# Kernel tuning notes

Hardware: AMD Instinct MI355X
Metric: run time of the kernel (lower is better)

Reference implementation:

```python
import jax, jax.numpy as jnp
import numpy as np

B, S, D, H, E = 2, 2048, 1024, 2048, 8
TOP_K = 2
AUX_COEF = 0.01


def setup_inputs() -> dict:
    key = jax.random.key(0)
    ks = jax.random.split(key, 5)
    x = jax.random.normal(ks[0], (B, S, D), jnp.float32)
    Wr = jax.random.normal(ks[1], (E, D), jnp.float32) * 0.02   # router: Linear(D, E) weight [E, D]
    W1 = jax.random.normal(ks[2], (E, H, D), jnp.float32) * 0.02  # per-expert Linear(D, H)
    W2 = jax.random.normal(ks[3], (E, D, H), jnp.float32) * 0.02  # per-expert Linear(H, D)
    W3 = jax.random.normal(ks[4], (E, H, D), jnp.float32) * 0.02  # per-expert Linear(D, H)
    return {"x": x, "Wr": Wr, "W1": W1, "W2": W2, "W3": W3}


def reference(x, Wr, W1, W2, W3):
    b, s, d = x.shape
    e = Wr.shape[0]
    xf = x.reshape(-1, d)                               # [N, D]
    logits = xf @ Wr.T                                  # [N, E]
    probs = jax.nn.softmax(logits, axis=-1)
    _, topk_idx = jax.lax.top_k(logits, TOP_K)          # indices from logits (as in torch code)
    topk_probs, _ = jax.lax.top_k(probs, TOP_K)         # values from probs (same order; softmax monotone)
    # aux loss: density of top-1 expert * mean router prob
    density = jnp.mean(jax.nn.one_hot(topk_idx[:, 0], e, dtype=xf.dtype), axis=0)
    aux_loss = AUX_COEF * jnp.sum(density * probs.mean(axis=0)) * e
    # combine gates: gate[n, j] = sum_i topk_probs[n,i] * 1[topk_idx[n,i]==j]
    gates = jnp.sum(jax.nn.one_hot(topk_idx, e, dtype=xf.dtype) * topk_probs[..., None], axis=1)  # [N, E]
    # dense per-expert SwiGLU; masked combine gives identical math to gather/scatter loop
    h = jax.nn.silu(jnp.einsum('nd,ehd->enh', xf, W1)) * jnp.einsum('nd,ehd->enh', xf, W3)  # [E, N, H]
    y = jnp.einsum('enh,edh->end', h, W2)               # [E, N, D]
    out = jnp.einsum('ne,end->nd', gates, y)            # [N, D]
    return out.reshape(b, s, d), aux_loss
```

## Files before the change

### kernel.cpp

```cpp
#include <hip/hip_runtime.h>
#include <stdint.h>

#define NTOK 4096
#define DD 1024
#define HH 2048
#define NE 8
#define CAP 4096

typedef short bf16x8 __attribute__((ext_vector_type(8)));
typedef float f32x4 __attribute__((ext_vector_type(4)));
typedef unsigned short u16;
typedef unsigned int u32;

__device__ __forceinline__ u16 f2b(float f){
    union { float f; u32 u; } v; v.f = f;
    return (u16)((v.u + 0x7fffu + ((v.u >> 16) & 1u)) >> 16);
}
__device__ __forceinline__ float b2f(u16 h){
    union { u32 u; float f; } v; v.u = ((u32)h) << 16;
    return v.f;
}
__device__ __forceinline__ u32 pk2(float a, float b){
    return (u32)f2b(a) | ((u32)f2b(b) << 16);
}
__device__ __forceinline__ void gload16(const u16* g, u16* l){
    __builtin_amdgcn_global_load_lds((const __attribute__((address_space(1))) u32*)g,
                                     (__attribute__((address_space(3))) u32*)l, 16, 0, 0);
}

__global__ __launch_bounds__(256) void prep_kernel(const float* __restrict__ x,
        const float* __restrict__ Wr,
        const float* __restrict__ W1, const float* __restrict__ W2, const float* __restrict__ W3,
        u16* __restrict__ xb, u16* __restrict__ w1b, u16* __restrict__ w2b, u16* __restrict__ w3b,
        int* __restrict__ cnt, int* __restrict__ list,
        float* __restrict__ glist, float* __restrict__ psum,
        int* __restrict__ cnt1, int* __restrict__ islot){
    __shared__ float wS[NE * DD];
    __shared__ float psumS[NE];
    __shared__ int cnt1S[NE], cntS[NE], baseS[NE];
    __shared__ int tE[32], tL[32];
    __shared__ float tP[32];
    int tid = threadIdx.x;
    int bid = blockIdx.x;

    if (bid >= 256){
        int cb = bid - 256;
        int m = cb >> 10, blk = cb & 1023;
        const float* s = (m == 0) ? W1 : (m == 1) ? W2 : W3;
        u16* d = (m == 0) ? w1b : (m == 1) ? w2b : w3b;
        int base = blk * 4096 + tid;
        #pragma unroll 4
        for (int j = 0; j < 16; ++j){
            int i = base + j * 256;
            float4 v = reinterpret_cast<const float4*>(s)[i];
            ushort4 o; o.x = f2b(v.x); o.y = f2b(v.y); o.z = f2b(v.z); o.w = f2b(v.w);
            reinterpret_cast<ushort4*>(d)[i] = o;
        }
        return;
    }

    for (int i = tid; i < NE * DD / 4; i += 256)
        reinterpret_cast<float4*>(wS)[i] = reinterpret_cast<const float4*>(Wr)[i];
    if (tid < NE){ psumS[tid] = 0.f; cnt1S[tid] = 0; cntS[tid] = 0; }
    __syncthreads();
    int lane = tid & 63, w = tid >> 6;
    for (int t = 0; t < 4; ++t){
        int li = w * 4 + t;
        int n = bid * 16 + li;
        const float4* xr = reinterpret_cast<const float4*>(x + (size_t)n * DD);
        ushort4* xbr = reinterpret_cast<ushort4*>(xb + (size_t)n * DD);
        float acc[NE];
        #pragma unroll
        for (int e = 0; e < NE; ++e) acc[e] = 0.f;
        #pragma unroll
        for (int j = 0; j < 4; ++j){
            float4 xv = xr[lane + 64 * j];
            ushort4 xo; xo.x = f2b(xv.x); xo.y = f2b(xv.y); xo.z = f2b(xv.z); xo.w = f2b(xv.w);
            xbr[lane + 64 * j] = xo;
            #pragma unroll
            for (int e = 0; e < NE; ++e){
                float4 wv = reinterpret_cast<const float4*>(wS + e * DD)[lane + 64 * j];
                acc[e] += xv.x * wv.x + xv.y * wv.y + xv.z * wv.z + xv.w * wv.w;
            }
        }
        #pragma unroll
        for (int e = 0; e < NE; ++e){
            float v = acc[e];
            #pragma unroll
            for (int s = 32; s > 0; s >>= 1) v += __shfl_xor(v, s);
            acc[e] = v;
        }
        if (lane == 0){
            float mx = acc[0];
            #pragma unroll
            for (int e = 1; e < NE; ++e) mx = fmaxf(mx, acc[e]);
            float p[NE], sm = 0.f;
            #pragma unroll
            for (int e = 0; e < NE; ++e){ p[e] = expf(acc[e] - mx); sm += p[e]; }
            float inv = 1.f / sm;
            #pragma unroll
            for (int e = 0; e < NE; ++e){ p[e] *= inv; atomicAdd(&psumS[e], p[e]); }
            int i0 = 0;
            #pragma unroll
            for (int e = 1; e < NE; ++e) if (acc[e] > acc[i0]) i0 = e;
            int i1 = -1;
            #pragma unroll
            for (int e = 0; e < NE; ++e) if (e != i0 && (i1 < 0 || acc[e] > acc[i1])) i1 = e;
            atomicAdd(&cnt1S[i0], 1);
            int l0 = atomicAdd(&cntS[i0], 1);
            int l1 = atomicAdd(&cntS[i1], 1);
            tE[li * 2] = i0; tE[li * 2 + 1] = i1;
            tP[li * 2] = p[i0]; tP[li * 2 + 1] = p[i1];
            tL[li * 2] = l0; tL[li * 2 + 1] = l1;
        }
    }
    __syncthreads();
    if (tid < NE){
        baseS[tid] = atomicAdd(&cnt[tid], cntS[tid]);
        atomicAdd(&psum[tid], psumS[tid]);
        atomicAdd(&cnt1[tid], cnt1S[tid]);
    }
    __syncthreads();
    if (tid < 32){
        int e = tE[tid], pos = baseS[e] + tL[tid];
        int n = bid * 16 + (tid >> 1);
        list[e * CAP + pos]  = n;
        glist[e * CAP + pos] = tP[tid];
        islot[n * 2 + (tid & 1)] = e * CAP + pos;
    }
}

__global__ void finalize_kernel(const int* __restrict__ cnt, int* __restrict__ offs,
                                const float* __restrict__ psum, const int* __restrict__ cnt1,
                                float* __restrict__ aux_out){
    if (threadIdx.x == 0 && blockIdx.x == 0){
        int o = 0; float aux = 0.f;
        for (int e = 0; e < NE; ++e){
            offs[e] = o; o += cnt[e];
            aux += ((float)cnt1[e] * (1.f / NTOK)) * (psum[e] * (1.f / NTOK));
        }
        aux_out[0] = 0.01f * aux * (float)NE;
    }
}

__global__ __launch_bounds__(256, 3) void ffn1_kernel(const u16* __restrict__ xb,
        const u16* __restrict__ w1b, const u16* __restrict__ w3b,
        const int* __restrict__ cnt, const int* __restrict__ offs,
        const int* __restrict__ list, u16* __restrict__ hbuf){
    int bid = blockIdx.x;
    int widx = (bid & 7) * 1024 + (bid >> 3);
    int e = widx >> 10, n0t = (widx >> 5) & 31, mt = widx & 31;
    int rows = cnt[e];
    int m0 = mt * 128;
    if (m0 >= rows) return;
    int n0 = n0t * 64;

    __shared__ u16 aS[128 * 64];
    __shared__ u16 bS[128 * 64];

    int tid = threadIdx.x, lane = tid & 63, w = tid >> 6;
    int wm = (w & 1) * 64, wn = (w >> 1) * 32;
    int fr = lane & 15, fg = lane >> 4, fr7 = fr & 7;
    int rc = lane >> 3, ce = ((lane & 7) ^ rc) * 8;

    const u16* aptr[4];
    const u16* bptr[4];
    #pragma unroll
    for (int q = 0; q < 4; ++q){
        int r = m0 + (w * 4 + q) * 8 + rc;
        int tok = list[e * CAP + (r < rows ? r : rows - 1)];
        aptr[q] = xb + (size_t)tok * DD + ce;
        int br = (w * 4 + q) * 8 + rc;
        const u16* wb = (br < 64) ? w1b : w3b;
        bptr[q] = wb + ((size_t)e * HH + n0 + (br & 63)) * DD + ce;
    }
    u16* aL = aS + w * 4 * 512;
    u16* bL = bS + w * 4 * 512;

    f32x4 acc1[4][2], acc3[4][2];
    #pragma unroll
    for (int mi = 0; mi < 4; ++mi)
        #pragma unroll
        for (int ni = 0; ni < 2; ++ni)
            #pragma unroll
            for (int j = 0; j < 4; ++j){ acc1[mi][ni][j] = 0.f; acc3[mi][ni][j] = 0.f; }

    for (int k0 = 0; k0 < DD; k0 += 64){
        #pragma unroll
        for (int q = 0; q < 4; ++q){
            gload16(aptr[q] + k0, aL + q * 512);
            gload16(bptr[q] + k0, bL + q * 512);
        }
        __syncthreads();
        #pragma unroll
        for (int ks = 0; ks < 2; ++ks){
            int sl = ((ks * 4 + fg) ^ fr7) * 8;
            bf16x8 a[4], b1[2], b3[2];
            #pragma unroll
            for (int mi = 0; mi < 4; ++mi)
                a[mi] = *reinterpret_cast<const bf16x8*>(&aS[(wm + mi * 16 + fr) * 64 + sl]);
            #pragma unroll
            for (int ni = 0; ni < 2; ++ni){
                b1[ni] = *reinterpret_cast<const bf16x8*>(&bS[(wn + ni * 16 + fr) * 64 + sl]);
                b3[ni] = *reinterpret_cast<const bf16x8*>(&bS[(64 + wn + ni * 16 + fr) * 64 + sl]);
            }
            #pragma unroll
            for (int mi = 0; mi < 4; ++mi)
                #pragma unroll
                for (int ni = 0; ni < 2; ++ni){
                    acc1[mi][ni] = __builtin_amdgcn_mfma_f32_16x16x32_bf16(a[mi], b1[ni], acc1[mi][ni], 0, 0, 0);
                    acc3[mi][ni] = __builtin_amdgcn_mfma_f32_16x16x32_bf16(a[mi], b3[ni], acc3[mi][ni], 0, 0, 0);
                }
        }
        __syncthreads();
    }

    int hoff = offs[e];
    #pragma unroll
    for (int mi = 0; mi < 4; ++mi)
        #pragma unroll
        for (int ni = 0; ni < 2; ++ni)
            #pragma unroll
            for (int j = 0; j < 4; ++j){
                int r = wm + mi * 16 + fg * 4 + j;
                int tr = m0 + r;
                if (tr < rows){
                    int c = n0 + wn + ni * 16 + fr;
                    float v1 = acc1[mi][ni][j], v3 = acc3[mi][ni][j];
                    float hv = (v1 / (1.f + expf(-v1))) * v3;
                    hbuf[(size_t)(hoff + tr) * HH + c] = f2b(hv);
                }
            }
}

__global__ __launch_bounds__(256, 3) void ffn2_kernel(const u16* __restrict__ hbuf,
        const u16* __restrict__ w2b, const int* __restrict__ cnt,
        const int* __restrict__ offs, u16* __restrict__ ybuf){
    int bid = blockIdx.x;
    int widx = (bid & 7) * 256 + (bid >> 3);
    int e = widx >> 8, n0t = (widx >> 5) & 7, mt = widx & 31;
    int rows = cnt[e];
    int m0 = mt * 128;
    if (m0 >= rows) return;
    int n0 = n0t * 128;

    __shared__ u16 aS[128 * 64];
    __shared__ u16 bS[128 * 64];

    int tid = threadIdx.x, lane = tid & 63, w = tid >> 6;
    int wm = (w & 1) * 64, wn = (w >> 1) * 64;
    int fr = lane & 15, fg = lane >> 4, fr7 = fr & 7;
    int rc = lane >> 3, ce = ((lane & 7) ^ rc) * 8;

    int hoff = offs[e];
    const u16* aptr[4];
    #pragma unroll
    for (int q = 0; q < 4; ++q){
        int r = m0 + (w * 4 + q) * 8 + rc;
        if (r >= rows) r = rows - 1;
        aptr[q] = hbuf + (size_t)(hoff + r) * HH + ce;
    }
    const u16* bp = w2b + ((size_t)e * DD + n0 + w * 32 + rc) * HH + ce;
    u16* aL = aS + w * 4 * 512;
    u16* bL = bS + w * 4 * 512;

    f32x4 acc[4][4];
    #pragma unroll
    for (int mi = 0; mi < 4; ++mi)
        #pragma unroll
        for (int ni = 0; ni < 4; ++ni)
            #pragma unroll
            for (int j = 0; j < 4; ++j) acc[mi][ni][j] = 0.f;

    for (int k0 = 0; k0 < HH; k0 += 64){
        #pragma unroll
        for (int q = 0; q < 4; ++q){
            gload16(aptr[q] + k0, aL + q * 512);
            gload16(bp + q * 8 * HH + k0, bL + q * 512);
        }
        __syncthreads();
        #pragma unroll
        for (int ks = 0; ks < 2; ++ks){
            int sl = ((ks * 4 + fg) ^ fr7) * 8;
            bf16x8 a[4], b[4];
            #pragma unroll
            for (int mi = 0; mi < 4; ++mi)
                a[mi] = *reinterpret_cast<const bf16x8*>(&aS[(wm + mi * 16 + fr) * 64 + sl]);
            #pragma unroll
            for (int ni = 0; ni < 4; ++ni)
                b[ni] = *reinterpret_cast<const bf16x8*>(&bS[(wn + ni * 16 + fr) * 64 + sl]);
            #pragma unroll
            for (int mi = 0; mi < 4; ++mi)
                #pragma unroll
                for (int ni = 0; ni < 4; ++ni)
                    acc[mi][ni] = __builtin_amdgcn_mfma_f32_16x16x32_bf16(a[mi], b[ni], acc[mi][ni], 0, 0, 0);
        }
        __syncthreads();
    }

    #pragma unroll
    for (int mi = 0; mi < 4; ++mi)
        #pragma unroll
        for (int ni = 0; ni < 4; ++ni)
            #pragma unroll
            for (int j = 0; j < 4; ++j){
                int r = wm + mi * 16 + fg * 4 + j;
                int tr = m0 + r;
                if (tr < rows){
                    int c = wn + ni * 16 + fr;
                    ybuf[(size_t)(hoff + tr) * DD + n0 + c] = f2b(acc[mi][ni][j]);
                }
            }
}

__global__ __launch_bounds__(256, 2) void ffn1_small(const u16* __restrict__ xb,
        const float* __restrict__ W1f, const float* __restrict__ W3f,
        const int* __restrict__ cnt, const int* __restrict__ offs,
        const int* __restrict__ list, u16* __restrict__ hbuf){
    int bid = blockIdx.x;
    int widx = (bid & 7) * 512 + (bid >> 3);
    int e = widx >> 9, n0t = (widx >> 5) & 15, mt = widx & 31;
    int rows = cnt[e];
    int m0 = mt * 128;
    if (m0 >= rows) return;
    int n0 = n0t * 128;
    __shared__ u16 aS[128 * 64];
    __shared__ u16 b1S[128 * 64];
    __shared__ u16 b3S[128 * 64];
    int tid = threadIdx.x, lane = tid & 63, w = tid >> 6;
    int wm = (w & 1) * 64, wn = (w >> 1) * 64;
    int fr = lane & 15, fg = lane >> 4, fr7 = fr & 7;
    int rc = lane >> 3, ce = ((lane & 7) ^ rc) * 8;
    const u16* aptr[4];
    #pragma unroll
    for (int q = 0; q < 4; ++q){
        int r = m0 + (w * 4 + q) * 8 + rc;
        int tok = list[e * CAP + (r < rows ? r : rows - 1)];
        aptr[q] = xb + (size_t)tok * DD + ce;
    }
    size_t brw = (size_t)(e * HH + n0 + w * 32 + rc) * DD + ce;
    const float* b1pf = W1f + brw;
    const float* b3pf = W3f + brw;
    u16* aL  = aS  + w * 4 * 512;
    u16* b1L = b1S + w * 4 * 512;
    u16* b3L = b3S + w * 4 * 512;
    f32x4 acc1[4][4], acc3[4][4];
    #pragma unroll
    for (int mi = 0; mi < 4; ++mi)
        #pragma unroll
        for (int ni = 0; ni < 4; ++ni)
            #pragma unroll
            for (int j = 0; j < 4; ++j){ acc1[mi][ni][j] = 0.f; acc3[mi][ni][j] = 0.f; }
    for (int k0 = 0; k0 < DD; k0 += 64){
        #pragma unroll
        for (int q = 0; q < 4; ++q){
            gload16(aptr[q] + k0, aL + q * 512);
            const float* s1 = b1pf + q * 8 * DD + k0;
            float4 f0 = reinterpret_cast<const float4*>(s1)[0];
            float4 f1 = reinterpret_cast<const float4*>(s1)[1];
            int4 v; v.x = pk2(f0.x,f0.y); v.y = pk2(f0.z,f0.w); v.z = pk2(f1.x,f1.y); v.w = pk2(f1.z,f1.w);
            *reinterpret_cast<int4*>(b1L + q * 512 + lane * 8) = v;
            const float* s3 = b3pf + q * 8 * DD + k0;
            float4 g0 = reinterpret_cast<const float4*>(s3)[0];
            float4 g1 = reinterpret_cast<const float4*>(s3)[1];
            int4 u; u.x = pk2(g0.x,g0.y); u.y = pk2(g0.z,g0.w); u.z = pk2(g1.x,g1.y); u.w = pk2(g1.z,g1.w);
            *reinterpret_cast<int4*>(b3L + q * 512 + lane * 8) = u;
        }
        __syncthreads();
        #pragma unroll
        for (int ks = 0; ks < 2; ++ks){
            int sl = ((ks * 4 + fg) ^ fr7) * 8;
            bf16x8 a[4], b1[4], b3[4];
            #pragma unroll
            for (int mi = 0; mi < 4; ++mi)
                a[mi] = *reinterpret_cast<const bf16x8*>(&aS[(wm + mi * 16 + fr) * 64 + sl]);
            #pragma unroll
            for (int ni = 0; ni < 4; ++ni){
                b1[ni] = *reinterpret_cast<const bf16x8*>(&b1S[(wn + ni * 16 + fr) * 64 + sl]);
                b3[ni] = *reinterpret_cast<const bf16x8*>(&b3S[(wn + ni * 16 + fr) * 64 + sl]);
            }
            #pragma unroll
            for (int mi = 0; mi < 4; ++mi)
                #pragma unroll
                for (int ni = 0; ni < 4; ++ni){
                    acc1[mi][ni] = __builtin_amdgcn_mfma_f32_16x16x32_bf16(a[mi], b1[ni], acc1[mi][ni], 0, 0, 0);
                    acc3[mi][ni] = __builtin_amdgcn_mfma_f32_16x16x32_bf16(a[mi], b3[ni], acc3[mi][ni], 0, 0, 0);
                }
        }
        __syncthreads();
    }
    int hoff = offs[e];
    #pragma unroll
    for (int mi = 0; mi < 4; ++mi)
        #pragma unroll
        for (int ni = 0; ni < 4; ++ni)
            #pragma unroll
            for (int j = 0; j < 4; ++j){
                int r = wm + mi * 16 + fg * 4 + j;
                int tr = m0 + r;
                if (tr < rows){
                    int c = wn + ni * 16 + fr;
                    float v1 = acc1[mi][ni][j], v3 = acc3[mi][ni][j];
                    float hv = (v1 / (1.f + expf(-v1))) * v3;
                    hbuf[(size_t)(hoff + tr) * HH + n0 + c] = f2b(hv);
                }
            }
}

__global__ __launch_bounds__(256, 2) void ffn2_small(const u16* __restrict__ hbuf,
        const float* __restrict__ W2f, const int* __restrict__ cnt,
        const int* __restrict__ offs, u16* __restrict__ ybuf){
    int bid = blockIdx.x;
    int widx = (bid & 7) * 256 + (bid >> 3);
    int e = widx >> 8, n0t = (widx >> 5) & 7, mt = widx & 31;
    int rows = cnt[e];
    int m0 = mt * 128;
    if (m0 >= rows) return;
    int n0 = n0t * 128;
    __shared__ u16 aS[128 * 64];
    __shared__ u16 bS[128 * 64];
    int tid = threadIdx.x, lane = tid & 63, w = tid >> 6;
    int wm = (w & 1) * 64, wn = (w >> 1) * 64;
    int fr = lane & 15, fg = lane >> 4, fr7 = fr & 7;
    int rc = lane >> 3, ce = ((lane & 7) ^ rc) * 8;
    int hoff = offs[e];
    const u16* aptr[4];
    #pragma unroll
    for (int q = 0; q < 4; ++q){
        int r = m0 + (w * 4 + q) * 8 + rc;
        if (r >= rows) r = rows - 1;
        aptr[q] = hbuf + (size_t)(hoff + r) * HH + ce;
    }
    const float* b2pf = W2f + (size_t)(e * DD + n0 + w * 32 + rc) * HH + ce;
    u16* aL = aS + w * 4 * 512;
    u16* bL = bS + w * 4 * 512;
    f32x4 acc[4][4];
    #pragma unroll
    for (int mi = 0; mi < 4; ++mi)
        #pragma unroll
        for (int ni = 0; ni < 4; ++ni)
            #pragma unroll
            for (int j = 0; j < 4; ++j) acc[mi][ni][j] = 0.f;
    for (int k0 = 0; k0 < HH; k0 += 64){
        #pragma unroll
        for (int q = 0; q < 4; ++q){
            gload16(aptr[q] + k0, aL + q * 512);
            const float* s2 = b2pf + q * 8 * HH + k0;
            float4 f0 = reinterpret_cast<const float4*>(s2)[0];
            float4 f1 = reinterpret_cast<const float4*>(s2)[1];
            int4 v; v.x = pk2(f0.x,f0.y); v.y = pk2(f0.z,f0.w); v.z = pk2(f1.x,f1.y); v.w = pk2(f1.z,f1.w);
            *reinterpret_cast<int4*>(bL + q * 512 + lane * 8) = v;
        }
        __syncthreads();
        #pragma unroll
        for (int ks = 0; ks < 2; ++ks){
            int sl = ((ks * 4 + fg) ^ fr7) * 8;
            bf16x8 a[4], b[4];
            #pragma unroll
            for (int mi = 0; mi < 4; ++mi)
                a[mi] = *reinterpret_cast<const bf16x8*>(&aS[(wm + mi * 16 + fr) * 64 + sl]);
            #pragma unroll
            for (int ni = 0; ni < 4; ++ni)
                b[ni] = *reinterpret_cast<const bf16x8*>(&bS[(wn + ni * 16 + fr) * 64 + sl]);
            #pragma unroll
            for (int mi = 0; mi < 4; ++mi)
                #pragma unroll
                for (int ni = 0; ni < 4; ++ni)
                    acc[mi][ni] = __builtin_amdgcn_mfma_f32_16x16x32_bf16(a[mi], b[ni], acc[mi][ni], 0, 0, 0);
        }
        __syncthreads();
    }
    #pragma unroll
    for (int mi = 0; mi < 4; ++mi)
        #pragma unroll
        for (int ni = 0; ni < 4; ++ni)
            #pragma unroll
            for (int j = 0; j < 4; ++j){
                int r = wm + mi * 16 + fg * 4 + j;
                int tr = m0 + r;
                if (tr < rows){
                    int c = wn + ni * 16 + fr;
                    ybuf[(size_t)(hoff + tr) * DD + n0 + c] = f2b(acc[mi][ni][j]);
                }
            }
}

__global__ __launch_bounds__(256) void combine_kernel(const u16* __restrict__ ybuf,
        const int* __restrict__ islot, const int* __restrict__ offs,
        const float* __restrict__ glist, float* __restrict__ out){
    int idx = blockIdx.x * 256 + threadIdx.x;
    int n = idx >> 7, c = (idx & 127) * 8;
    int id0 = islot[n * 2], id1 = islot[n * 2 + 1];
    int r0 = offs[id0 >> 12] + (id0 & 4095);
    int r1 = offs[id1 >> 12] + (id1 & 4095);
    float g0 = glist[id0], g1 = glist[id1];
    ushort4 y0a = reinterpret_cast<const ushort4*>(ybuf + (size_t)r0 * DD + c)[0];
    ushort4 y0b = reinterpret_cast<const ushort4*>(ybuf + (size_t)r0 * DD + c)[1];
    ushort4 y1a = reinterpret_cast<const ushort4*>(ybuf + (size_t)r1 * DD + c)[0];
    ushort4 y1b = reinterpret_cast<const ushort4*>(ybuf + (size_t)r1 * DD + c)[1];
    float4 o0, o1;
    o0.x = g0 * b2f(y0a.x) + g1 * b2f(y1a.x);
    o0.y = g0 * b2f(y0a.y) + g1 * b2f(y1a.y);
    o0.z = g0 * b2f(y0a.z) + g1 * b2f(y1a.z);
    o0.w = g0 * b2f(y0a.w) + g1 * b2f(y1a.w);
    o1.x = g0 * b2f(y0b.x) + g1 * b2f(y1b.x);
    o1.y = g0 * b2f(y0b.y) + g1 * b2f(y1b.y);
    o1.z = g0 * b2f(y0b.z) + g1 * b2f(y1b.z);
    o1.w = g0 * b2f(y0b.w) + g1 * b2f(y1b.w);
    float4* op = reinterpret_cast<float4*>(out + (size_t)n * DD + c);
    op[0] = o0; op[1] = o1;
}

extern "C" void kernel_launch(void* const* d_in, const int* in_sizes, int n_in,
                              void* d_out, int out_size, void* d_ws, size_t ws_size,
                              hipStream_t stream) {
    const float* x  = (const float*)d_in[0];
    const float* Wr = (const float*)d_in[1];
    const float* W1 = (const float*)d_in[2];
    const float* W2 = (const float*)d_in[3];
    const float* W3 = (const float*)d_in[4];
    float* out = (float*)d_out;

    char* wp = (char*)d_ws;
    u16*   hbuf  = (u16*)  (wp);
    u16*   xb    = (u16*)  (wp + 33554432);
    int*   list  = (int*)  (wp + 41943040);
    float* glist = (float*)(wp + 42074112);
    int*   cnt   = (int*)  (wp + 42205184);
    int*   offs  = (int*)  (wp + 42205216);
    float* psum  = (float*)(wp + 42205248);
    int*   cnt1  = (int*)  (wp + 42205280);
    int*   islot = (int*)  (wp + 42205312);
    const size_t WOFF = 42238208;
    const size_t WB   = 33554432;
    u16* w1b = (u16*)(wp + WOFF);
    u16* w2b = (u16*)(wp + WOFF + WB);
    u16* w3b = (u16*)(wp + WOFF + 2 * WB);
    u16* ybuf = (u16*)(wp + WOFF);
    const size_t NEED_FULL = WOFF + 3 * WB;
    bool bw = ws_size >= NEED_FULL;

    hipMemsetAsync(wp + 42205184, 0, 128, stream);

    prep_kernel<<<bw ? 3328 : 256, 256, 0, stream>>>(
        x, Wr, W1, W2, W3, xb, w1b, w2b, w3b, cnt, list, glist, psum, cnt1, islot);
    finalize_kernel<<<1, 64, 0, stream>>>(cnt, offs, psum, cnt1, out + (size_t)NTOK * DD);
    if (bw){
        ffn1_kernel<<<8192, 256, 0, stream>>>(xb, w1b, w3b, cnt, offs, list, hbuf);
        ffn2_kernel<<<2048, 256, 0, stream>>>(hbuf, w2b, cnt, offs, ybuf);
    } else {
        ffn1_small<<<4096, 256, 0, stream>>>(xb, W1, W3, cnt, offs, list, hbuf);
        ffn2_small<<<2048, 256, 0, stream>>>(hbuf, W2, cnt, offs, ybuf);
    }
    combine_kernel<<<NTOK * (DD / 8) / 256, 256, 0, stream>>>(ybuf, islot, offs, glist, out);
}
```

Baseline: 221.3 us.

## Drop finalize kernel and make ffn1 a persistent grid over M tiles

Removes the single-thread finalize launch: expert offsets are now recomputed inline from counts in each kernel, and the aux loss is written by the first thread of the combine kernel. ffn1 now launches 768 blocks (8 experts × 32 N-tiles × 3), and each block strides over M tiles of its expert instead of launching one block per tile, many of which exited early. This cuts a launch and the idle blocks, but load balance now depends on the per-expert token counts: a single block may process many M tiles serially.

Result: faster. 209.5 us (-5.3%).

```diff
diff --git a/kernel.cpp b/kernel.cpp
--- a/kernel.cpp
+++ b/kernel.cpp
@@ -26,6 +26,12 @@
 __device__ __forceinline__ void gload16(const u16* g, u16* l){
     __builtin_amdgcn_global_load_lds((const __attribute__((address_space(1))) u32*)g,
                                      (__attribute__((address_space(3))) u32*)l, 16, 0, 0);
+}
+__device__ __forceinline__ int prefix_off(const int* __restrict__ cnt, int e){
+    int o = 0;
+    #pragma unroll
+    for (int i = 0; i < NE; ++i) if (i < e) o += cnt[i];
+    return o;
 }
 
 __global__ __launch_bounds__(256) void prep_kernel(const float* __restrict__ x,
@@ -130,30 +136,16 @@
     }
 }
 
-__global__ void finalize_kernel(const int* __restrict__ cnt, int* __restrict__ offs,
-                                const float* __restrict__ psum, const int* __restrict__ cnt1,
-                                float* __restrict__ aux_out){
-    if (threadIdx.x == 0 && blockIdx.x == 0){
-        int o = 0; float aux = 0.f;
-        for (int e = 0; e < NE; ++e){
-            offs[e] = o; o += cnt[e];
-            aux += ((float)cnt1[e] * (1.f / NTOK)) * (psum[e] * (1.f / NTOK));
-        }
-        aux_out[0] = 0.01f * aux * (float)NE;
-    }
-}
-
 __global__ __launch_bounds__(256, 3) void ffn1_kernel(const u16* __restrict__ xb,
         const u16* __restrict__ w1b, const u16* __restrict__ w3b,
-        const int* __restrict__ cnt, const int* __restrict__ offs,
-        const int* __restrict__ list, u16* __restrict__ hbuf){
+        const int* __restrict__ cnt, const int* __restrict__ list,
+        u16* __restrict__ hbuf){
     int bid = blockIdx.x;
-    int widx = (bid & 7) * 1024 + (bid >> 3);
-    int e = widx >> 10, n0t = (widx >> 5) & 31, mt = widx & 31;
+    int e = bid & 7;
+    int slot = bid >> 3;
     int rows = cnt[e];
-    int m0 = mt * 128;
-    if (m0 >= rows) return;
-    int n0 = n0t * 64;
+    int hoff = prefix_off(cnt, e);
+    int n0 = (slot & 31) * 64;
 
     __shared__ u16 aS[128 * 64];
     __shared__ u16 bS[128 * 64];
@@ -163,13 +155,9 @@
     int fr = lane & 15, fg = lane >> 4, fr7 = fr & 7;
     int rc = lane >> 3, ce = ((lane & 7) ^ rc) * 8;
 
-    const u16* aptr[4];
     const u16* bptr[4];
     #pragma unroll
     for (int q = 0; q < 4; ++q){
-        int r = m0 + (w * 4 + q) * 8 + rc;
-        int tok = list[e * CAP + (r < rows ? r : rows - 1)];
-        aptr[q] = xb + (size_t)tok * DD + ce;
         int br = (w * 4 + q) * 8 + rc;
         const u16* wb = (br < 64) ? w1b : w3b;
         bptr[q] = wb + ((size_t)e * HH + n0 + (br & 63)) * DD + ce;
@@ -177,65 +165,77 @@
     u16* aL = aS + w * 4 * 512;
     u16* bL = bS + w * 4 * 512;
 
-    f32x4 acc1[4][2], acc3[4][2];
-    #pragma unroll
-    for (int mi = 0; mi < 4; ++mi)
-        #pragma unroll
-        for (int ni = 0; ni < 2; ++ni)
-            #pragma unroll
-            for (int j = 0; j < 4; ++j){ acc1[mi][ni][j] = 0.f; acc3[mi][ni][j] = 0.f; }
-
-    for (int k0 = 0; k0 < DD; k0 += 64){
+    for (int mt = slot >> 5; mt < 32; mt += 3){
+        int m0 = mt << 7;
+        if (m0 >= rows) break;
+
+        const u16* aptr[4];
         #pragma unroll
         for (int q = 0; q < 4; ++q){
-            gload16(aptr[q] + k0, aL + q * 512);
-            gload16(bptr[q] + k0, bL + q * 512);
-        }
-        __syncthreads();
-        #pragma unroll
-        for (int ks = 0; ks < 2; ++ks){
-            int sl = ((ks * 4 + fg) ^ fr7) * 8;
-            bf16x8 a[4], b1[2], b3[2];
-            #pragma unroll
-            for (int mi = 0; mi < 4; ++mi)
-                a[mi] = *reinterpret_cast<const bf16x8*>(&aS[(wm + mi * 16 + fr) * 64 + sl]);
-            #pragma unroll
-            for (int ni = 0; ni < 2; ++ni){
-                b1[ni] = *reinterpret_cast<const bf16x8*>(&bS[(wn + ni * 16 + fr) * 64 + sl]);
-                b3[ni] = *reinterpret_cast<const bf16x8*>(&bS[(64 + wn + ni * 16 + fr) * 64 + sl]);
-            }
-            #pragma unroll
-            for (int mi = 0; mi < 4; ++mi)
+            int r = m0 + (w * 4 + q) * 8 + rc;
+            int tok = list[e * CAP + (r < rows ? r : rows - 1)];
+            aptr[q] = xb + (size_t)tok * DD + ce;
+        }
+
+        f32x4 acc1[4][2], acc3[4][2];
+        #pragma unroll
+        for (int mi = 0; mi < 4; ++mi)
+            #pragma unroll
+            for (int ni = 0; ni < 2; ++ni)
+                #pragma unroll
+                for (int j = 0; j < 4; ++j){ acc1[mi][ni][j] = 0.f; acc3[mi][ni][j] = 0.f; }
+
+        for (int k0 = 0; k0 < DD; k0 += 64){
+            #pragma unroll
+            for (int q = 0; q < 4; ++q){
+                gload16(aptr[q] + k0, aL + q * 512);
+                gload16(bptr[q] + k0, bL + q * 512);
+            }
+            __syncthreads();
+            #pragma unroll
+            for (int ks = 0; ks < 2; ++ks){
+                int sl = ((ks * 4 + fg) ^ fr7) * 8;
+                bf16x8 a[4], b1[2], b3[2];
+                #pragma unroll
+                for (int mi = 0; mi < 4; ++mi)
+                    a[mi] = *reinterpret_cast<const bf16x8*>(&aS[(wm + mi * 16 + fr) * 64 + sl]);
                 #pragma unroll
                 for (int ni = 0; ni < 2; ++ni){
-                    acc1[mi][ni] = __builtin_amdgcn_mfma_f32_16x16x32_bf16(a[mi], b1[ni], acc1[mi][ni], 0, 0, 0);
-                    acc3[mi][ni] = __builtin_amdgcn_mfma_f32_16x16x32_bf16(a[mi], b3[ni], acc3[mi][ni], 0, 0, 0);
+                    b1[ni] = *reinterpret_cast<const bf16x8*>(&bS[(wn + ni * 16 + fr) * 64 + sl]);
+                    b3[ni] = *reinterpret_cast<const bf16x8*>(&bS[(64 + wn + ni * 16 + fr) * 64 + sl]);
                 }
-        }
-        __syncthreads();
-    }
-
-    int hoff = offs[e];
-    #pragma unroll
-    for (int mi = 0; mi < 4; ++mi)
-        #pragma unroll
-        for (int ni = 0; ni < 2; ++ni)
-            #pragma unroll
-            for (int j = 0; j < 4; ++j){
-                int r = wm + mi * 16 + fg * 4 + j;
-                int tr = m0 + r;
-                if (tr < rows){
-                    int c = n0 + wn + ni * 16 + fr;
-                    float v1 = acc1[mi][ni][j], v3 = acc3[mi][ni][j];
-                    float hv = (v1 / (1.f + expf(-v1))) * v3;
-                    hbuf[(size_t)(hoff + tr) * HH + c] = f2b(hv);
+                #pragma unroll
+                for (int mi = 0; mi < 4; ++mi)
+                    #pragma unroll
+                    for (int ni = 0; ni < 2; ++ni){
+                        acc1[mi][ni] = __builtin_amdgcn_mfma_f32_16x16x32_bf16(a[mi], b1[ni], acc1[mi][ni], 0, 0, 0);
+                        acc3[mi][ni] = __builtin_amdgcn_mfma_f32_16x16x32_bf16(a[mi], b3[ni], acc3[mi][ni], 0, 0, 0);
+                    }
+            }
+            __syncthreads();
+        }
+
+        #pragma unroll
+        for (int mi = 0; mi < 4; ++mi)
+            #pragma unroll
+            for (int ni = 0; ni < 2; ++ni)
+                #pragma unroll
+                for (int j = 0; j < 4; ++j){
+                    int r = wm + mi * 16 + fg * 4 + j;
+                    int tr = m0 + r;
+                    if (tr < rows){
+                        int c = n0 + wn + ni * 16 + fr;
+                        float v1 = acc1[mi][ni][j], v3 = acc3[mi][ni][j];
+                        float hv = (v1 / (1.f + expf(-v1))) * v3;
+                        hbuf[(size_t)(hoff + tr) * HH + c] = f2b(hv);
+                    }
                 }
-            }
+    }
 }
 
 __global__ __launch_bounds__(256, 3) void ffn2_kernel(const u16* __restrict__ hbuf,
         const u16* __restrict__ w2b, const int* __restrict__ cnt,
-        const int* __restrict__ offs, u16* __restrict__ ybuf){
+        u16* __restrict__ ybuf){
     int bid = blockIdx.x;
     int widx = (bid & 7) * 256 + (bid >> 3);
     int e = widx >> 8, n0t = (widx >> 5) & 7, mt = widx & 31;
@@ -243,6 +243,7 @@
     int m0 = mt * 128;
     if (m0 >= rows) return;
     int n0 = n0t * 128;
+    int hoff = prefix_off(cnt, e);
 
     __shared__ u16 aS[128 * 64];
     __shared__ u16 bS[128 * 64];
@@ -252,7 +253,6 @@
     int fr = lane & 15, fg = lane >> 4, fr7 = fr & 7;
     int rc = lane >> 3, ce = ((lane & 7) ^ rc) * 8;
 
-    int hoff = offs[e];
     const u16* aptr[4];
     #pragma unroll
     for (int q = 0; q < 4; ++q){
@@ -315,8 +315,8 @@
 
 __global__ __launch_bounds__(256, 2) void ffn1_small(const u16* __restrict__ xb,
         const float* __restrict__ W1f, const float* __restrict__ W3f,
-        const int* __restrict__ cnt, const int* __restrict__ offs,
-        const int* __restrict__ list, u16* __restrict__ hbuf){
+        const int* __restrict__ cnt, const int* __restrict__ list,
+        u16* __restrict__ hbuf){
     int bid = blockIdx.x;
     int widx = (bid & 7) * 512 + (bid >> 3);
     int e = widx >> 9, n0t = (widx >> 5) & 15, mt = widx & 31;
@@ -324,6 +324,7 @@
     int m0 = mt * 128;
     if (m0 >= rows) return;
     int n0 = n0t * 128;
+    int hoff = prefix_off(cnt, e);
     __shared__ u16 aS[128 * 64];
     __shared__ u16 b1S[128 * 64];
     __shared__ u16 b3S[128 * 64];
@@ -389,7 +390,6 @@
         }
         __syncthreads();
     }
-    int hoff = offs[e];
     #pragma unroll
     for (int mi = 0; mi < 4; ++mi)
         #pragma unroll
@@ -409,7 +409,7 @@
 
 __global__ __launch_bounds__(256, 2) void ffn2_small(const u16* __restrict__ hbuf,
         const float* __restrict__ W2f, const int* __restrict__ cnt,
-        const int* __restrict__ offs, u16* __restrict__ ybuf){
+        u16* __restrict__ ybuf){
     int bid = blockIdx.x;
     int widx = (bid & 7) * 256 + (bid >> 3);
     int e = widx >> 8, n0t = (widx >> 5) & 7, mt = widx & 31;
@@ -417,13 +417,13 @@
     int m0 = mt * 128;
     if (m0 >= rows) return;
     int n0 = n0t * 128;
+    int hoff = prefix_off(cnt, e);
     __shared__ u16 aS[128 * 64];
     __shared__ u16 bS[128 * 64];
     int tid = threadIdx.x, lane = tid & 63, w = tid >> 6;
     int wm = (w & 1) * 64, wn = (w >> 1) * 64;
     int fr = lane & 15, fg = lane >> 4, fr7 = fr & 7;
     int rc = lane >> 3, ce = ((lane & 7) ^ rc) * 8;
-    int hoff = offs[e];
     const u16* aptr[4];
     #pragma unroll
     for (int q = 0; q < 4; ++q){
@@ -486,13 +486,21 @@
 }
 
 __global__ __launch_bounds__(256) void combine_kernel(const u16* __restrict__ ybuf,
-        const int* __restrict__ islot, const int* __restrict__ offs,
-        const float* __restrict__ glist, float* __restrict__ out){
+        const int* __restrict__ islot, const int* __restrict__ cnt,
+        const float* __restrict__ glist, const float* __restrict__ psum,
+        const int* __restrict__ cnt1, float* __restrict__ out){
     int idx = blockIdx.x * 256 + threadIdx.x;
+    if (idx == 0){
+        float aux = 0.f;
+        #pragma unroll
+        for (int e = 0; e < NE; ++e)
+            aux += ((float)cnt1[e] * (1.f / NTOK)) * (psum[e] * (1.f / NTOK));
+        out[(size_t)NTOK * DD] = 0.01f * aux * (float)NE;
+    }
     int n = idx >> 7, c = (idx & 127) * 8;
     int id0 = islot[n * 2], id1 = islot[n * 2 + 1];
-    int r0 = offs[id0 >> 12] + (id0 & 4095);
-    int r1 = offs[id1 >> 12] + (id1 & 4095);
+    int r0 = prefix_off(cnt, id0 >> 12) + (id0 & 4095);
+    int r1 = prefix_off(cnt, id1 >> 12) + (id1 & 4095);
     float g0 = glist[id0], g1 = glist[id1];
     ushort4 y0a = reinterpret_cast<const ushort4*>(ybuf + (size_t)r0 * DD + c)[0];
     ushort4 y0b = reinterpret_cast<const ushort4*>(ybuf + (size_t)r0 * DD + c)[1];
@@ -527,9 +535,8 @@
     int*   list  = (int*)  (wp + 41943040);
     float* glist = (float*)(wp + 42074112);
     int*   cnt   = (int*)  (wp + 42205184);
-    int*   offs  = (int*)  (wp + 42205216);
-    float* psum  = (float*)(wp + 42205248);
-    int*   cnt1  = (int*)  (wp + 42205280);
+    float* psum  = (float*)(wp + 42205216);
+    int*   cnt1  = (int*)  (wp + 42205248);
     int*   islot = (int*)  (wp + 42205312);
     const size_t WOFF = 42238208;
     const size_t WB   = 33554432;
@@ -544,13 +551,13 @@
 
     prep_kernel<<<bw ? 3328 : 256, 256, 0, stream>>>(
         x, Wr, W1, W2, W3, xb, w1b, w2b, w3b, cnt, list, glist, psum, cnt1, islot);
-    finalize_kernel<<<1, 64, 0, stream>>>(cnt, offs, psum, cnt1, out + (size_t)NTOK * DD);
     if (bw){
-        ffn1_kernel<<<8192, 256, 0, stream>>>(xb, w1b, w3b, cnt, offs, list, hbuf);
-        ffn2_kernel<<<2048, 256, 0, stream>>>(hbuf, w2b, cnt, offs, ybuf);
+        ffn1_kernel<<<768, 256, 0, stream>>>(xb, w1b, w3b, cnt, list, hbuf);
+        ffn2_kernel<<<2048, 256, 0, stream>>>(hbuf, w2b, cnt, ybuf);
     } else {
-        ffn1_small<<<4096, 256, 0, stream>>>(xb, W1, W3, cnt, offs, list, hbuf);
-        ffn2_small<<<2048, 256, 0, stream>>>(hbuf, W2, cnt, offs, ybuf);
-    }
-    combine_kernel<<<NTOK * (DD / 8) / 256, 256, 0, stream>>>(ybuf, islot, offs, glist, out);
-}
+        ffn1_small<<<4096, 256, 0, stream>>>(xb, W1, W3, cnt, list, hbuf);
+        ffn2_small<<<2048, 256, 0, stream>>>(hbuf, W2, cnt, ybuf);
+    }
+    combine_kernel<<<NTOK * (DD / 8) / 256, 256, 0, stream>>>(
+        ybuf, islot, cnt, glist, psum, cnt1, out);
+}
```
